# Kernel tuning notes

Measured on AMD Instinct MI355X. Metric: run time of the kernel, lower is better.

Reference implementation:

```python
import jax, jax.numpy as jnp
import numpy as np

D = 1024      # model_dim
DK = 1024     # keys_dim
DV = 1024     # values_dim
H = 16        # heads
HDK = DK // H # per-head key dim (64)
HDV = DV // H
FF = 2048     # FFN default hidden_dim
EPS = 1e-5


def setup_inputs() -> dict:
    key = jax.random.key(0)
    ks = jax.random.split(key, 16)
    s = lambda k, sh, fan: jax.random.normal(k, sh, jnp.float32) * (1.0 / np.sqrt(fan))
    return {
        "x": jax.random.normal(ks[0], (8, 1024, D), jnp.float32),
        # per-head projections stored as [D, H, hd] (concat of the H small Linears)
        "Wq": s(ks[1], (D, H, HDK), D), "bq": jnp.zeros((H, HDK), jnp.float32),
        "Wk": s(ks[2], (D, H, HDK), D), "bk": jnp.zeros((H, HDK), jnp.float32),
        "Wv": s(ks[3], (D, H, HDV), D), "bv": jnp.zeros((H, HDV), jnp.float32),
        "Wo": s(ks[4], (DV, D), DV), "bo": jnp.zeros((D,), jnp.float32),
        "ln1_g": jnp.ones((D,), jnp.float32), "ln1_b": jnp.zeros((D,), jnp.float32),
        "W1": s(ks[5], (D, FF), D), "b1": jnp.zeros((FF,), jnp.float32),
        "W2": s(ks[6], (FF, D), FF), "b2": jnp.zeros((D,), jnp.float32),
        "ln2_g": jnp.ones((D,), jnp.float32), "ln2_b": jnp.zeros((D,), jnp.float32),
    }


def layer_norm(x, g, b):
    mu = jnp.mean(x, axis=-1, keepdims=True)
    var = jnp.mean(jnp.square(x - mu), axis=-1, keepdims=True)
    return (x - mu) * jax.lax.rsqrt(var + EPS) * g + b


def reference(x, Wq, bq, Wk, bk, Wv, bv, Wo, bo, ln1_g, ln1_b, W1, b1, W2, b2, ln2_g, ln2_b):
    # per-head projections (equivalent to H small Linears, batched)
    q = jnp.einsum("bsd,dhk->bhsk", x, Wq) + bq[:, None, :]
    k = jnp.einsum("bsd,dhk->bhsk", x, Wk) + bk[:, None, :]
    v = jnp.einsum("bsd,dhv->bhsv", x, Wv) + bv[:, None, :]
    # scaled dot-product attention per head (scale uses per-head dk)
    scores = jnp.einsum("bhsk,bhtk->bhst", q, k) / jnp.sqrt(jnp.float32(HDK))
    w = jax.nn.softmax(scores, axis=-1)
    ctx = jnp.einsum("bhst,bhtv->bhsv", w, v)           # [B,H,S,hdv]
    B, _, S, _ = ctx.shape
    ctx = ctx.transpose(0, 2, 1, 3).reshape(B, S, DV)   # concat heads
    c = ctx @ Wo + bo
    h = layer_norm(x + c, ln1_g, ln1_b)
    y = jax.nn.relu(h @ W1 + b1) @ W2 + b2
    return layer_norm(h + y, ln2_g, ln2_b)
```

## Files before the change

### kernel.cpp

```cpp
#include <hip/hip_runtime.h>
#include <hip/hip_bf16.h>
#include <cstdint>

typedef __bf16 bf16_t;
typedef __bf16 bf16x8 __attribute__((ext_vector_type(8)));
typedef __bf16 bf16x4 __attribute__((ext_vector_type(4)));
typedef float f32x4 __attribute__((ext_vector_type(4)));

#define SEQ    1024
#define BATCH  8
#define NTOK   8192
#define DMODEL 1024
#define NHEAD  16
#define HD     64
#define FFDIM  2048

__device__ __forceinline__ void async16(const void* g, void* l) {
  __builtin_amdgcn_global_load_lds(
      (const __attribute__((address_space(1))) void*)g,
      (__attribute__((address_space(3))) void*)l, 16, 0, 0);
}

__global__ __launch_bounds__(256)
void cast_bf16_kernel(const float* __restrict__ in, bf16_t* __restrict__ out, int n4) {
  int i = blockIdx.x * 256 + threadIdx.x;
  if (i >= n4) return;
  float4 v = ((const float4*)in)[i];
  bf16x4 o = { (bf16_t)v.x, (bf16_t)v.y, (bf16_t)v.z, (bf16_t)v.w };
  *(bf16x4*)&out[(size_t)i * 4] = o;
}

__global__ __launch_bounds__(256)
void transpose_cast_kernel(const float* __restrict__ W, bf16_t* __restrict__ Wt,
                           int R, int C) {
  __shared__ float tile[32][33];
  const int bx = blockIdx.x * 32;
  const int by = blockIdx.y * 32;
  const int tx = threadIdx.x;
  const int ty = threadIdx.y;
#pragma unroll
  for (int i = 0; i < 4; ++i)
    tile[ty + 8 * i][tx] = W[(size_t)(by + ty + 8 * i) * C + bx + tx];
  __syncthreads();
#pragma unroll
  for (int i = 0; i < 4; ++i)
    Wt[(size_t)(bx + ty + 8 * i) * R + by + tx] = (bf16_t)tile[tx][ty + 8 * i];
}

template <int EPI>
__global__ __launch_bounds__(256, 4)
void gemm_bt(const bf16_t* __restrict__ A, const bf16_t* __restrict__ Bt,
             const float* __restrict__ bias0, const float* __restrict__ bias1,
             const float* __restrict__ bias2,
             const float* __restrict__ residF, const bf16_t* __restrict__ residB,
             void* __restrict__ o0, void* __restrict__ o1, void* __restrict__ o2,
             int K, int ldo, float qscale) {
  __shared__ bf16_t As[8192];
  __shared__ bf16_t Bs[8192];
  const int tid = threadIdx.x, w = tid >> 6, l = tid & 63;
  const int fr = l & 15, kg = (l >> 4) * 8;
  const int bm = blockIdx.x << 7, bn = blockIdx.y << 7;
  const int wr = (w >> 1) * 64, wc = (w & 1) * 64;

  const int srow = l >> 3;
  const int scol = ((l & 7) ^ srow) * 8;
  const int xork = (fr & 7) << 3;

  f32x4 acc[4][4];
#pragma unroll
  for (int i = 0; i < 4; ++i)
#pragma unroll
    for (int j = 0; j < 4; ++j) acc[i][j] = (f32x4){0.f, 0.f, 0.f, 0.f};

  const bf16_t* Ab = A + (size_t)bm * K;
  const bf16_t* Bb = Bt + (size_t)bn * K;

  const int nk = K >> 6;
  for (int kt = 0; kt < nk; ++kt) {
    const int k0 = kt << 6;
#pragma unroll
    for (int j = 0; j < 4; ++j) {
      const int ch = w * 4 + j;
      const int row = ch * 8 + srow;
      async16(Ab + (size_t)row * K + k0 + scol, &As[ch * 512]);
      async16(Bb + (size_t)row * K + k0 + scol, &Bs[ch * 512]);
    }
    asm volatile("s_waitcnt vmcnt(0)" ::: "memory");
    __syncthreads();

#pragma unroll
    for (int kk = 0; kk < 2; ++kk) {
      bf16x8 a[4], b[4];
      const int ko = (kk * 32 + kg) ^ xork;
#pragma unroll
      for (int i = 0; i < 4; ++i)
        a[i] = *(const bf16x8*)&As[(wr + i * 16 + fr) * 64 + ko];
#pragma unroll
      for (int j = 0; j < 4; ++j)
        b[j] = *(const bf16x8*)&Bs[(wc + j * 16 + fr) * 64 + ko];
#pragma unroll
      for (int i = 0; i < 4; ++i)
#pragma unroll
        for (int j = 0; j < 4; ++j)
          acc[i][j] = __builtin_amdgcn_mfma_f32_16x16x32_bf16(a[i], b[j], acc[i][j], 0, 0, 0);
    }
    __syncthreads();
  }

  const int lr = (l >> 4) * 4, lc = fr;
#pragma unroll
  for (int j = 0; j < 4; ++j) {
    const int col = bn + wc + j * 16 + lc;
#pragma unroll
    for (int i = 0; i < 4; ++i) {
#pragma unroll
      for (int r = 0; r < 4; ++r) {
        const int row = bm + wr + i * 16 + lr + r;
        const float v = acc[i][j][r];
        if (EPI == 0) {
          float o = v + bias0[col];
          if (residF) o += residF[(size_t)row * ldo + col];
          ((float*)o0)[(size_t)row * ldo + col] = o;
        } else if (EPI == 3) {
          const size_t idx = (size_t)row * ldo + col;
          ((float*)o0)[idx] = v + bias0[col] + (float)residB[idx];
        } else if (EPI == 1) {
          ((bf16_t*)o0)[(size_t)row * ldo + col] = (bf16_t)fmaxf(v + bias0[col], 0.f);
        } else {
          const int mode = col >> 10, cl = col & 1023;
          const int b_ = row >> 10, s_ = row & 1023, h_ = cl >> 6, e_ = cl & 63;
          if (mode == 0) {
            ((bf16_t*)o0)[((size_t)((b_ * NHEAD + h_) * SEQ + s_)) * HD + e_] =
                (bf16_t)((v + bias0[cl]) * qscale);
          } else if (mode == 1) {
            ((bf16_t*)o1)[((size_t)((b_ * NHEAD + h_) * SEQ + s_)) * HD + e_] =
                (bf16_t)(v + bias1[cl]);
          } else {
            ((bf16_t*)o2)[((size_t)((b_ * NHEAD + h_) * HD + e_)) * SEQ + s_] =
                (bf16_t)(v + bias2[cl]);
          }
        }
      }
    }
  }
}

__global__ __launch_bounds__(256)
void attn_kernel(const bf16_t* __restrict__ Q, const bf16_t* __restrict__ K,
                 const bf16_t* __restrict__ VT, bf16_t* __restrict__ CTX) {
  const int bh = blockIdx.x;
  const int qt = blockIdx.y * 128;
  const int b_ = bh >> 4, h_ = bh & 15;
  const bf16_t* qh = Q + (size_t)bh * SEQ * HD;
  const bf16_t* kh = K + (size_t)bh * SEQ * HD;
  const bf16_t* vh = VT + (size_t)bh * HD * SEQ;
  const int tid = threadIdx.x, wave = tid >> 6, lane = tid & 63;
  const int fr = lane & 15, kg = (lane >> 4) * 8;
  const int lr = (lane >> 4) * 4, lc = lane & 15;

  __shared__ bf16_t Ks[2][64 * 64];
  __shared__ bf16_t Vs[2][64 * 64];
  __shared__ bf16_t Ps[128 * 64];

  const int srow = lane >> 3;
  const int scol = ((lane & 7) ^ srow) * 8;

  bf16x8 qf[2][2];
#pragma unroll
  for (int i = 0; i < 2; ++i)
#pragma unroll
    for (int kk = 0; kk < 2; ++kk)
      qf[i][kk] = *(const bf16x8*)&qh[(size_t)(qt + wave * 32 + i * 16 + fr) * HD + kk * 32 + kg];

  f32x4 octx[2][4];
  float mrun[2][4], lrun[2][4];
#pragma unroll
  for (int i = 0; i < 2; ++i)
#pragma unroll
    for (int j = 0; j < 4; ++j) octx[i][j] = (f32x4){0.f, 0.f, 0.f, 0.f};
#pragma unroll
  for (int i = 0; i < 2; ++i)
#pragma unroll
    for (int r = 0; r < 4; ++r) { mrun[i][r] = -1e30f; lrun[i][r] = 0.f; }

  auto stage = [&](int buf, int t) {
#pragma unroll
    for (int i = 0; i < 2; ++i) {
      const int ch = i * 4 + wave;
      const int row = ch * 8 + srow;
      async16(&kh[(size_t)(t * 64 + row) * HD + scol], &Ks[buf][ch * 512]);
      async16(&vh[(size_t)row * SEQ + t * 64 + scol], &Vs[buf][ch * 512]);
    }
  };

  stage(0, 0);
  asm volatile("s_waitcnt vmcnt(0)" ::: "memory");
  __syncthreads();

  for (int t = 0; t < SEQ / 64; ++t) {
    const int cur = t & 1;
    if (t + 1 < SEQ / 64) stage(cur ^ 1, t + 1);

    f32x4 sc[2][4];
#pragma unroll
    for (int i = 0; i < 2; ++i)
#pragma unroll
      for (int j = 0; j < 4; ++j) sc[i][j] = (f32x4){0.f, 0.f, 0.f, 0.f};
#pragma unroll
    for (int kk = 0; kk < 2; ++kk) {
      bf16x8 kf[4];
#pragma unroll
      for (int j = 0; j < 4; ++j) {
        const int row = j * 16 + fr;
        kf[j] = *(const bf16x8*)&Ks[cur][row * 64 + ((kk * 32 + kg) ^ ((row & 7) << 3))];
      }
#pragma unroll
      for (int i = 0; i < 2; ++i)
#pragma unroll
        for (int j = 0; j < 4; ++j)
          sc[i][j] = __builtin_amdgcn_mfma_f32_16x16x32_bf16(qf[i][kk], kf[j], sc[i][j], 0, 0, 0);
    }

    float pmx[2][4];
    int ok = 1;
#pragma unroll
    for (int i = 0; i < 2; ++i)
#pragma unroll
      for (int r = 0; r < 4; ++r) {
        const float m3 = fmaxf(fmaxf(sc[i][0][r], sc[i][1][r]),
                               fmaxf(sc[i][2][r], sc[i][3][r]));
        pmx[i][r] = m3;
        ok &= (m3 <= mrun[i][r] + 8.f) ? 1 : 0;
      }
    if (!__all(ok)) {
#pragma unroll
      for (int i = 0; i < 2; ++i)
#pragma unroll
        for (int r = 0; r < 4; ++r) {
          float mx = pmx[i][r];
#pragma unroll
          for (int m = 1; m < 16; m <<= 1) mx = fmaxf(mx, __shfl_xor(mx, m));
          const float mnew = fmaxf(mrun[i][r], mx);
          const float alpha = exp2f(mrun[i][r] - mnew);
          mrun[i][r] = mnew;
          lrun[i][r] *= alpha;
#pragma unroll
          for (int j = 0; j < 4; ++j) octx[i][j][r] *= alpha;
        }
    }
#pragma unroll
    for (int i = 0; i < 2; ++i)
#pragma unroll
      for (int r = 0; r < 4; ++r) {
        const float m = mrun[i][r];
        float s = 0.f;
#pragma unroll
        for (int j = 0; j < 4; ++j) {
          const float p = exp2f(sc[i][j][r] - m);
          sc[i][j][r] = p;
          s += p;
        }
        lrun[i][r] += s;
        const int prow = wave * 32 + i * 16 + lr + r;
#pragma unroll
        for (int j = 0; j < 4; ++j)
          Ps[prow * 64 + (((j * 16 + lc)) ^ ((prow & 7) << 3))] = (bf16_t)sc[i][j][r];
      }
    asm volatile("s_waitcnt lgkmcnt(0)" ::: "memory");

#pragma unroll
    for (int kk = 0; kk < 2; ++kk) {
      bf16x8 pf[2], vf[4];
#pragma unroll
      for (int i = 0; i < 2; ++i) {
        const int row = wave * 32 + i * 16 + fr;
        pf[i] = *(const bf16x8*)&Ps[row * 64 + ((kk * 32 + kg) ^ ((row & 7) << 3))];
      }
#pragma unroll
      for (int j = 0; j < 4; ++j) {
        const int row = j * 16 + fr;
        vf[j] = *(const bf16x8*)&Vs[cur][row * 64 + ((kk * 32 + kg) ^ ((row & 7) << 3))];
      }
#pragma unroll
      for (int i = 0; i < 2; ++i)
#pragma unroll
        for (int j = 0; j < 4; ++j)
          octx[i][j] = __builtin_amdgcn_mfma_f32_16x16x32_bf16(pf[i], vf[j], octx[i][j], 0, 0, 0);
    }

    asm volatile("s_waitcnt vmcnt(0)" ::: "memory");
    __syncthreads();
  }

#pragma unroll
  for (int i = 0; i < 2; ++i)
#pragma unroll
    for (int r = 0; r < 4; ++r) {
      float lsum = lrun[i][r];
#pragma unroll
      for (int m = 1; m < 16; m <<= 1) lsum += __shfl_xor(lsum, m);
      const float inv = 1.f / lsum;
      const int row = qt + wave * 32 + i * 16 + lr + r;
#pragma unroll
      for (int j = 0; j < 4; ++j) {
        const int c = j * 16 + lc;
        CTX[((size_t)(b_ * SEQ + row)) * DMODEL + h_ * HD + c] = (bf16_t)(octx[i][j][r] * inv);
      }
    }
}

template <int OUTB>
__global__ __launch_bounds__(256)
void ln_kernel(const float* __restrict__ Y, const float* __restrict__ g,
               const float* __restrict__ b, void* __restrict__ outp) {
  const int row = blockIdx.x, tid = threadIdx.x;
  const int wave = tid >> 6, lane = tid & 63;
  const float4 yv = ((const float4*)Y)[(size_t)row * 256 + tid];
  const float s0 = yv.x, s1 = yv.y, s2 = yv.z, s3 = yv.w;
  float sum = s0 + s1 + s2 + s3;
  float sq = s0 * s0 + s1 * s1 + s2 * s2 + s3 * s3;
#pragma unroll
  for (int off = 1; off < 64; off <<= 1) {
    sum += __shfl_xor(sum, off);
    sq += __shfl_xor(sq, off);
  }
  __shared__ float red[8];
  if (lane == 0) { red[wave] = sum; red[4 + wave] = sq; }
  __syncthreads();
  sum = red[0] + red[1] + red[2] + red[3];
  sq = red[4] + red[5] + red[6] + red[7];
  const float mu = sum * (1.f / 1024.f);
  const float var = sq * (1.f / 1024.f) - mu * mu;
  const float rstd = rsqrtf(var + 1e-5f);
  const float4 gv = ((const float4*)g)[tid];
  const float4 bv = ((const float4*)b)[tid];
  const float o0 = (s0 - mu) * rstd * gv.x + bv.x;
  const float o1 = (s1 - mu) * rstd * gv.y + bv.y;
  const float o2 = (s2 - mu) * rstd * gv.z + bv.z;
  const float o3 = (s3 - mu) * rstd * gv.w + bv.w;
  if (OUTB) {
    bf16x4 ob = { (bf16_t)o0, (bf16_t)o1, (bf16_t)o2, (bf16_t)o3 };
    *(bf16x4*)&((bf16_t*)outp)[(size_t)row * 1024 + tid * 4] = ob;
  } else {
    ((float4*)outp)[(size_t)row * 256 + tid] = make_float4(o0, o1, o2, o3);
  }
}

extern "C" void kernel_launch(void* const* d_in, const int* in_sizes, int n_in,
                              void* d_out, int out_size, void* d_ws, size_t ws_size,
                              hipStream_t stream) {
  const float* x   = (const float*)d_in[0];
  const float* Wq  = (const float*)d_in[1];
  const float* bq  = (const float*)d_in[2];
  const float* Wk  = (const float*)d_in[3];
  const float* bk  = (const float*)d_in[4];
  const float* Wv  = (const float*)d_in[5];
  const float* bv  = (const float*)d_in[6];
  const float* Wo  = (const float*)d_in[7];
  const float* bo  = (const float*)d_in[8];
  const float* g1  = (const float*)d_in[9];
  const float* be1 = (const float*)d_in[10];
  const float* W1  = (const float*)d_in[11];
  const float* b1  = (const float*)d_in[12];
  const float* W2  = (const float*)d_in[13];
  const float* b2  = (const float*)d_in[14];
  const float* g2  = (const float*)d_in[15];
  const float* be2 = (const float*)d_in[16];

  char* ws = (char*)d_ws;
  const size_t MB = 1u << 20;
  bf16_t* xb    = (bf16_t*)(ws + 0 * MB);
  bf16_t* WqkvT = (bf16_t*)(ws + 16 * MB);
  bf16_t* WoT   = (bf16_t*)(ws + 22 * MB);
  bf16_t* W1T   = (bf16_t*)(ws + 24 * MB);
  bf16_t* W2T   = (bf16_t*)(ws + 28 * MB);
  bf16_t* qb    = (bf16_t*)(ws + 32 * MB);
  bf16_t* kb    = (bf16_t*)(ws + 48 * MB);
  bf16_t* vT    = (bf16_t*)(ws + 64 * MB);
  float*  y0    = (float*)(ws + 80 * MB);
  bf16_t* ctx = xb;
  bf16_t* hb  = qb;
  bf16_t* u   = kb;

  cast_bf16_kernel<<<dim3(NTOK * DMODEL / 4 / 256), dim3(256), 0, stream>>>(x, xb, NTOK * DMODEL / 4);
  transpose_cast_kernel<<<dim3(32, 32), dim3(32, 8), 0, stream>>>(Wq, WqkvT, 1024, 1024);
  transpose_cast_kernel<<<dim3(32, 32), dim3(32, 8), 0, stream>>>(Wk, WqkvT + 1024 * 1024, 1024, 1024);
  transpose_cast_kernel<<<dim3(32, 32), dim3(32, 8), 0, stream>>>(Wv, WqkvT + 2 * 1024 * 1024, 1024, 1024);
  transpose_cast_kernel<<<dim3(32, 32), dim3(32, 8), 0, stream>>>(Wo, WoT, 1024, 1024);
  transpose_cast_kernel<<<dim3(64, 32), dim3(32, 8), 0, stream>>>(W1, W1T, 1024, 2048);
  transpose_cast_kernel<<<dim3(32, 64), dim3(32, 8), 0, stream>>>(W2, W2T, 2048, 1024);

  const float qscale = 0.125f * 1.44269504088896f;

  gemm_bt<2><<<dim3(64, 24), dim3(256), 0, stream>>>(
      xb, WqkvT, bq, bk, bv, nullptr, nullptr, qb, kb, vT, 1024, 0, qscale);

  attn_kernel<<<dim3(128, 8), dim3(256), 0, stream>>>(qb, kb, vT, ctx);

  gemm_bt<0><<<dim3(64, 8), dim3(256), 0, stream>>>(
      ctx, WoT, bo, nullptr, nullptr, x, nullptr, y0, nullptr, nullptr, 1024, 1024, 1.f);

  ln_kernel<1><<<dim3(NTOK), dim3(256), 0, stream>>>(y0, g1, be1, hb);

  gemm_bt<1><<<dim3(64, 16), dim3(256), 0, stream>>>(
      hb, W1T, b1, nullptr, nullptr, nullptr, nullptr, u, nullptr, nullptr, 1024, 2048, 1.f);

  gemm_bt<3><<<dim3(64, 8), dim3(256), 0, stream>>>(
      u, W2T, b2, nullptr, nullptr, nullptr, hb, y0, nullptr, nullptr, 2048, 1024, 1.f);

  ln_kernel<0><<<dim3(NTOK), dim3(256), 0, stream>>>(y0, g2, be2, (float*)d_out);
}
```

Measured before the change: 348.4 us.

## Load K and V fragments directly from global memory in attention kernel

Removes the double-buffered async LDS staging of K and V tiles and the per-iteration block barrier, so each wave reads its K and V MFMA fragments straight from global memory (relying on L1/L2 for reuse across waves). The V fragments are issued early, before the softmax, to hide latency. This cuts LDS traffic and synchronisation but multiplies global and cache load requests by the four waves sharing each tile. Ps stays in LDS and is private to each wave.

Result: slower. 381.2 us (+9.4%).

```diff
diff --git a/kernel.cpp b/kernel.cpp
--- a/kernel.cpp
+++ b/kernel.cpp
@@ -158,12 +158,7 @@
   const int fr = lane & 15, kg = (lane >> 4) * 8;
   const int lr = (lane >> 4) * 4, lc = lane & 15;
 
-  __shared__ bf16_t Ks[2][64 * 64];
-  __shared__ bf16_t Vs[2][64 * 64];
   __shared__ bf16_t Ps[128 * 64];
-
-  const int srow = lane >> 3;
-  const int scol = ((lane & 7) ^ srow) * 8;
 
   bf16x8 qf[2][2];
 #pragma unroll
@@ -183,24 +178,7 @@
 #pragma unroll
     for (int r = 0; r < 4; ++r) { mrun[i][r] = -1e30f; lrun[i][r] = 0.f; }
 
-  auto stage = [&](int buf, int t) {
-#pragma unroll
-    for (int i = 0; i < 2; ++i) {
-      const int ch = i * 4 + wave;
-      const int row = ch * 8 + srow;
-      async16(&kh[(size_t)(t * 64 + row) * HD + scol], &Ks[buf][ch * 512]);
-      async16(&vh[(size_t)row * SEQ + t * 64 + scol], &Vs[buf][ch * 512]);
-    }
-  };
-
-  stage(0, 0);
-  asm volatile("s_waitcnt vmcnt(0)" ::: "memory");
-  __syncthreads();
-
   for (int t = 0; t < SEQ / 64; ++t) {
-    const int cur = t & 1;
-    if (t + 1 < SEQ / 64) stage(cur ^ 1, t + 1);
-
     f32x4 sc[2][4];
 #pragma unroll
     for (int i = 0; i < 2; ++i)
@@ -210,16 +188,21 @@
     for (int kk = 0; kk < 2; ++kk) {
       bf16x8 kf[4];
 #pragma unroll
-      for (int j = 0; j < 4; ++j) {
-        const int row = j * 16 + fr;
-        kf[j] = *(const bf16x8*)&Ks[cur][row * 64 + ((kk * 32 + kg) ^ ((row & 7) << 3))];
-      }
+      for (int j = 0; j < 4; ++j)
+        kf[j] = *(const bf16x8*)&kh[(size_t)(t * 64 + j * 16 + fr) * HD + kk * 32 + kg];
 #pragma unroll
       for (int i = 0; i < 2; ++i)
 #pragma unroll
         for (int j = 0; j < 4; ++j)
           sc[i][j] = __builtin_amdgcn_mfma_f32_16x16x32_bf16(qf[i][kk], kf[j], sc[i][j], 0, 0, 0);
     }
+
+    bf16x8 vf[2][4];
+#pragma unroll
+    for (int kk = 0; kk < 2; ++kk)
+#pragma unroll
+      for (int j = 0; j < 4; ++j)
+        vf[kk][j] = *(const bf16x8*)&vh[(size_t)(j * 16 + fr) * SEQ + t * 64 + kk * 32 + kg];
 
     float pmx[2][4];
     int ok = 1;
@@ -270,26 +253,18 @@
 
 #pragma unroll
     for (int kk = 0; kk < 2; ++kk) {
-      bf16x8 pf[2], vf[4];
+      bf16x8 pf[2];
 #pragma unroll
       for (int i = 0; i < 2; ++i) {
         const int row = wave * 32 + i * 16 + fr;
         pf[i] = *(const bf16x8*)&Ps[row * 64 + ((kk * 32 + kg) ^ ((row & 7) << 3))];
       }
 #pragma unroll
-      for (int j = 0; j < 4; ++j) {
-        const int row = j * 16 + fr;
-        vf[j] = *(const bf16x8*)&Vs[cur][row * 64 + ((kk * 32 + kg) ^ ((row & 7) << 3))];
-      }
-#pragma unroll
       for (int i = 0; i < 2; ++i)
 #pragma unroll
         for (int j = 0; j < 4; ++j)
-          octx[i][j] = __builtin_amdgcn_mfma_f32_16x16x32_bf16(pf[i], vf[j], octx[i][j], 0, 0, 0);
-    }
-
-    asm volatile("s_waitcnt vmcnt(0)" ::: "memory");
-    __syncthreads();
+          octx[i][j] = __builtin_amdgcn_mfma_f32_16x16x32_bf16(pf[i], vf[kk][j], octx[i][j], 0, 0, 0);
+    }
   }
 
 #pragma unroll
```

## Keep attention probabilities in registers via transposed MFMA and lane shuffles

Applied to the files above, without the earlier changes.

Swaps the MFMA operand order so the score tiles come out transposed, with each lane holding one query row. This makes the row max and sum reductions mostly in-lane, needing only two cross-lane shuffles. The probabilities are packed to bf16 and redistributed with __shfl into the B-operand layout for the PV MFMA, which removes the LDS round-trip through the Ps buffer and its wait. It also adds a min-blocks hint of 4 to launch bounds and vectorizes the context store, at the cost of extra shuffle instructions and possible register pressure.

Result: faster. 340.3 us (-2.3%).

```diff
diff --git a/kernel.cpp b/kernel.cpp
--- a/kernel.cpp
+++ b/kernel.cpp
@@ -19,6 +19,12 @@
   __builtin_amdgcn_global_load_lds(
       (const __attribute__((address_space(1))) void*)g,
       (__attribute__((address_space(3))) void*)l, 16, 0, 0);
+}
+
+__device__ __forceinline__ uint32_t pack2bf(float a, float b) {
+  union { bf16_t h[2]; uint32_t u; } t;
+  t.h[0] = (bf16_t)a; t.h[1] = (bf16_t)b;
+  return t.u;
 }
 
 __global__ __launch_bounds__(256)
@@ -145,7 +151,7 @@
   }
 }
 
-__global__ __launch_bounds__(256)
+__global__ __launch_bounds__(256, 4)
 void attn_kernel(const bf16_t* __restrict__ Q, const bf16_t* __restrict__ K,
                  const bf16_t* __restrict__ VT, bf16_t* __restrict__ CTX) {
   const int bh = blockIdx.x;
@@ -155,12 +161,10 @@
   const bf16_t* kh = K + (size_t)bh * SEQ * HD;
   const bf16_t* vh = VT + (size_t)bh * HD * SEQ;
   const int tid = threadIdx.x, wave = tid >> 6, lane = tid & 63;
-  const int fr = lane & 15, kg = (lane >> 4) * 8;
-  const int lr = (lane >> 4) * 4, lc = lane & 15;
+  const int fr = lane & 15, g = lane >> 4, kg = g * 8;
 
   __shared__ bf16_t Ks[2][64 * 64];
   __shared__ bf16_t Vs[2][64 * 64];
-  __shared__ bf16_t Ps[128 * 64];
 
   const int srow = lane >> 3;
   const int scol = ((lane & 7) ^ srow) * 8;
@@ -173,15 +177,13 @@
       qf[i][kk] = *(const bf16x8*)&qh[(size_t)(qt + wave * 32 + i * 16 + fr) * HD + kk * 32 + kg];
 
   f32x4 octx[2][4];
-  float mrun[2][4], lrun[2][4];
-#pragma unroll
-  for (int i = 0; i < 2; ++i)
+  float mrun[2], lrun[2];
+#pragma unroll
+  for (int i = 0; i < 2; ++i) {
 #pragma unroll
     for (int j = 0; j < 4; ++j) octx[i][j] = (f32x4){0.f, 0.f, 0.f, 0.f};
-#pragma unroll
-  for (int i = 0; i < 2; ++i)
-#pragma unroll
-    for (int r = 0; r < 4; ++r) { mrun[i][r] = -1e30f; lrun[i][r] = 0.f; }
+    mrun[i] = -1e30f; lrun[i] = 0.f;
+  }
 
   auto stage = [&](int buf, int t) {
 #pragma unroll
@@ -197,6 +199,10 @@
   asm volatile("s_waitcnt vmcnt(0)" ::: "memory");
   __syncthreads();
 
+  const int srcA = fr + ((g & 1) << 5);
+  const int srcB = srcA + 16;
+  const bool ghi = (g >= 2);
+
   for (int t = 0; t < SEQ / 64; ++t) {
     const int cur = t & 1;
     if (t + 1 < SEQ / 64) stage(cur ^ 1, t + 1);
@@ -218,74 +224,79 @@
       for (int i = 0; i < 2; ++i)
 #pragma unroll
         for (int j = 0; j < 4; ++j)
-          sc[i][j] = __builtin_amdgcn_mfma_f32_16x16x32_bf16(qf[i][kk], kf[j], sc[i][j], 0, 0, 0);
-    }
-
-    float pmx[2][4];
+          sc[i][j] = __builtin_amdgcn_mfma_f32_16x16x32_bf16(kf[j], qf[i][kk], sc[i][j], 0, 0, 0);
+    }
+
+    float pmx[2];
     int ok = 1;
 #pragma unroll
-    for (int i = 0; i < 2; ++i)
-#pragma unroll
-      for (int r = 0; r < 4; ++r) {
-        const float m3 = fmaxf(fmaxf(sc[i][0][r], sc[i][1][r]),
-                               fmaxf(sc[i][2][r], sc[i][3][r]));
-        pmx[i][r] = m3;
-        ok &= (m3 <= mrun[i][r] + 8.f) ? 1 : 0;
-      }
+    for (int i = 0; i < 2; ++i) {
+      float m0 = fmaxf(fmaxf(sc[i][0][0], sc[i][0][1]), fmaxf(sc[i][0][2], sc[i][0][3]));
+      float m1 = fmaxf(fmaxf(sc[i][1][0], sc[i][1][1]), fmaxf(sc[i][1][2], sc[i][1][3]));
+      float m2 = fmaxf(fmaxf(sc[i][2][0], sc[i][2][1]), fmaxf(sc[i][2][2], sc[i][2][3]));
+      float m3 = fmaxf(fmaxf(sc[i][3][0], sc[i][3][1]), fmaxf(sc[i][3][2], sc[i][3][3]));
+      pmx[i] = fmaxf(fmaxf(m0, m1), fmaxf(m2, m3));
+      ok &= (pmx[i] <= mrun[i] + 8.f) ? 1 : 0;
+    }
     if (!__all(ok)) {
 #pragma unroll
-      for (int i = 0; i < 2; ++i)
+      for (int i = 0; i < 2; ++i) {
+        float mx = pmx[i];
+        mx = fmaxf(mx, __shfl_xor(mx, 16));
+        mx = fmaxf(mx, __shfl_xor(mx, 32));
+        const float mnew = fmaxf(mrun[i], mx);
+        const float alpha = exp2f(mrun[i] - mnew);
+        mrun[i] = mnew;
+        lrun[i] *= alpha;
+#pragma unroll
+        for (int j = 0; j < 4; ++j)
+#pragma unroll
+          for (int r = 0; r < 4; ++r) octx[i][j][r] *= alpha;
+      }
+    }
+    uint32_t pk[2][4][2];
+#pragma unroll
+    for (int i = 0; i < 2; ++i) {
+      const float m = mrun[i];
+      float s = 0.f;
+#pragma unroll
+      for (int j = 0; j < 4; ++j) {
 #pragma unroll
         for (int r = 0; r < 4; ++r) {
-          float mx = pmx[i][r];
-#pragma unroll
-          for (int m = 1; m < 16; m <<= 1) mx = fmaxf(mx, __shfl_xor(mx, m));
-          const float mnew = fmaxf(mrun[i][r], mx);
-          const float alpha = exp2f(mrun[i][r] - mnew);
-          mrun[i][r] = mnew;
-          lrun[i][r] *= alpha;
-#pragma unroll
-          for (int j = 0; j < 4; ++j) octx[i][j][r] *= alpha;
-        }
-    }
-#pragma unroll
-    for (int i = 0; i < 2; ++i)
-#pragma unroll
-      for (int r = 0; r < 4; ++r) {
-        const float m = mrun[i][r];
-        float s = 0.f;
-#pragma unroll
-        for (int j = 0; j < 4; ++j) {
           const float p = exp2f(sc[i][j][r] - m);
           sc[i][j][r] = p;
           s += p;
         }
-        lrun[i][r] += s;
-        const int prow = wave * 32 + i * 16 + lr + r;
-#pragma unroll
-        for (int j = 0; j < 4; ++j)
-          Ps[prow * 64 + (((j * 16 + lc)) ^ ((prow & 7) << 3))] = (bf16_t)sc[i][j][r];
-      }
-    asm volatile("s_waitcnt lgkmcnt(0)" ::: "memory");
-
-#pragma unroll
-    for (int kk = 0; kk < 2; ++kk) {
-      bf16x8 pf[2], vf[4];
+        pk[i][j][0] = pack2bf(sc[i][j][0], sc[i][j][1]);
+        pk[i][j][1] = pack2bf(sc[i][j][2], sc[i][j][3]);
+      }
+      lrun[i] += s;
+    }
+
+#pragma unroll
+    for (int kk2 = 0; kk2 < 2; ++kk2) {
+      bf16x8 vf[4];
+#pragma unroll
+      for (int j2 = 0; j2 < 4; ++j2) {
+        const int row = j2 * 16 + fr;
+        vf[j2] = *(const bf16x8*)&Vs[cur][row * 64 + ((kk2 * 32 + kg) ^ ((row & 7) << 3))];
+      }
+      const int jlo = 2 * kk2, jhi = jlo + 1;
 #pragma unroll
       for (int i = 0; i < 2; ++i) {
-        const int row = wave * 32 + i * 16 + fr;
-        pf[i] = *(const bf16x8*)&Ps[row * 64 + ((kk * 32 + kg) ^ ((row & 7) << 3))];
-      }
-#pragma unroll
-      for (int j = 0; j < 4; ++j) {
-        const int row = j * 16 + fr;
-        vf[j] = *(const bf16x8*)&Vs[cur][row * 64 + ((kk * 32 + kg) ^ ((row & 7) << 3))];
-      }
-#pragma unroll
-      for (int i = 0; i < 2; ++i)
-#pragma unroll
-        for (int j = 0; j < 4; ++j)
-          octx[i][j] = __builtin_amdgcn_mfma_f32_16x16x32_bf16(pf[i], vf[j], octx[i][j], 0, 0, 0);
+        const uint32_t aL0 = __shfl(pk[i][jlo][0], srcA), aL1 = __shfl(pk[i][jlo][1], srcA);
+        const uint32_t bL0 = __shfl(pk[i][jlo][0], srcB), bL1 = __shfl(pk[i][jlo][1], srcB);
+        const uint32_t aH0 = __shfl(pk[i][jhi][0], srcA), aH1 = __shfl(pk[i][jhi][1], srcA);
+        const uint32_t bH0 = __shfl(pk[i][jhi][0], srcB), bH1 = __shfl(pk[i][jhi][1], srcB);
+        union { bf16x8 v; uint32_t u[4]; } pf;
+        pf.u[0] = ghi ? aH0 : aL0;
+        pf.u[1] = ghi ? aH1 : aL1;
+        pf.u[2] = ghi ? bH0 : bL0;
+        pf.u[3] = ghi ? bH1 : bL1;
+#pragma unroll
+        for (int j2 = 0; j2 < 4; ++j2)
+          octx[i][j2] = __builtin_amdgcn_mfma_f32_16x16x32_bf16(vf[j2], pf.v, octx[i][j2], 0, 0, 0);
+      }
     }
 
     asm volatile("s_waitcnt vmcnt(0)" ::: "memory");
@@ -293,20 +304,20 @@
   }
 
 #pragma unroll
-  for (int i = 0; i < 2; ++i)
-#pragma unroll
-    for (int r = 0; r < 4; ++r) {
-      float lsum = lrun[i][r];
-#pragma unroll
-      for (int m = 1; m < 16; m <<= 1) lsum += __shfl_xor(lsum, m);
-      const float inv = 1.f / lsum;
-      const int row = qt + wave * 32 + i * 16 + lr + r;
-#pragma unroll
-      for (int j = 0; j < 4; ++j) {
-        const int c = j * 16 + lc;
-        CTX[((size_t)(b_ * SEQ + row)) * DMODEL + h_ * HD + c] = (bf16_t)(octx[i][j][r] * inv);
-      }
-    }
+  for (int i = 0; i < 2; ++i) {
+    float lsum = lrun[i];
+    lsum += __shfl_xor(lsum, 16);
+    lsum += __shfl_xor(lsum, 32);
+    const float inv = 1.f / lsum;
+    const int row = qt + wave * 32 + i * 16 + fr;
+    const size_t base = ((size_t)(b_ * SEQ + row)) * DMODEL + h_ * HD;
+#pragma unroll
+    for (int j2 = 0; j2 < 4; ++j2) {
+      bf16x4 o = { (bf16_t)(octx[i][j2][0] * inv), (bf16_t)(octx[i][j2][1] * inv),
+                   (bf16_t)(octx[i][j2][2] * inv), (bf16_t)(octx[i][j2][3] * inv) };
+      *(bf16x4*)&CTX[base + j2 * 16 + g * 4] = o;
+    }
+  }
 }
 
 template <int OUTB>
```
